# Kernel tuning notes

Measured on AMD Instinct MI355X. Metric: run time of the kernel, lower is better.

Reference implementation:

```python
import jax, jax.numpy as jnp
import numpy as np

V, D, NL = 50257, 768, 12
DI, DS, DC, DTR = 1536, 16, 4, 48  # d_inner, d_state, d_conv, dt_rank
B, S = 2, 1024


def _mamba_layer(x, iw, cw, cb, xw, dw, db, Alog, Dp, ow):
    # x: (B,S,D)
    xz = x @ iw.T                      # (B,S,2*DI)
    xin, z = jnp.split(xz, 2, axis=-1)
    # depthwise causal conv over sequence
    xc = jax.lax.conv_general_dilated(
        jnp.transpose(xin, (0, 2, 1)), cw[:, None, :],
        window_strides=(1,), padding=[(DC - 1, 0)],
        feature_group_count=DI, dimension_numbers=('NCL', 'OIL', 'NCL'))
    xin = jax.nn.silu(jnp.transpose(xc, (0, 2, 1)) + cb)  # (B,S,DI)
    dbl = xin @ xw.T                   # (B,S,DTR+2*DS)
    dt, Bm, Cm = dbl[..., :DTR], dbl[..., DTR:DTR + DS], dbl[..., DTR + DS:]
    dt = jax.nn.softplus(dt @ dw.T + db)  # (B,S,DI)
    A = -jnp.exp(Alog)                 # (DI,DS)

    def step(h, inp):
        dt_t, B_t, C_t, x_t = inp      # (B,DI),(B,DS),(B,DS),(B,DI)
        h = h * jnp.exp(dt_t[:, :, None] * A) + (dt_t * x_t)[:, :, None] * B_t[:, None, :]
        y = jnp.einsum('bds,bs->bd', h, C_t)
        return h, y

    h0 = jnp.zeros((x.shape[0], DI, DS), dtype=x.dtype)
    xs = (jnp.transpose(dt, (1, 0, 2)), jnp.transpose(Bm, (1, 0, 2)),
          jnp.transpose(Cm, (1, 0, 2)), jnp.transpose(xin, (1, 0, 2)))
    _, ys = jax.lax.scan(step, h0, xs)
    y = jnp.transpose(ys, (1, 0, 2)) + xin * Dp  # (B,S,DI)
    y = y * jax.nn.silu(z)
    return y @ ow.T                    # (B,S,D)


def _layernorm(x, w, b):
    mu = jnp.mean(x, axis=-1, keepdims=True)
    var = jnp.mean(jnp.square(x - mu), axis=-1, keepdims=True)
    return (x - mu) * jax.lax.rsqrt(var + 1e-5) * w + b


def setup_inputs() -> dict:
    key = jax.random.key(0)
    ks = jax.random.split(key, 10)
    s = 0.02
    input_ids = jax.random.randint(ks[0], (B, S), 0, V)
    emb = jax.random.normal(ks[1], (V, D), jnp.float32) * s
    in_proj_w = jax.random.normal(ks[2], (NL, 2 * DI, D), jnp.float32) * s
    conv_w = jax.random.normal(ks[3], (NL, DI, DC), jnp.float32) * 0.2
    conv_b = jnp.zeros((NL, DI), jnp.float32)
    x_proj_w = jax.random.normal(ks[4], (NL, DTR + 2 * DS, DI), jnp.float32) * s
    dt_proj_w = jax.random.normal(ks[5], (NL, DI, DTR), jnp.float32) * (DTR ** -0.5)
    dt_proj_b = jax.random.normal(ks[6], (NL, DI), jnp.float32) * 0.1 - 4.0
    A_log = jnp.broadcast_to(jnp.log(jnp.arange(1, DS + 1, dtype=jnp.float32)), (NL, DI, DS)) + 0.0
    D_param = jnp.ones((NL, DI), jnp.float32)
    out_proj_w = jax.random.normal(ks[7], (NL, D, DI), jnp.float32) * s
    norm_w = jnp.ones((D,), jnp.float32)
    norm_b = jnp.zeros((D,), jnp.float32)
    return {"input_ids": input_ids, "emb": emb, "in_proj_w": in_proj_w,
            "conv_w": conv_w, "conv_b": conv_b, "x_proj_w": x_proj_w,
            "dt_proj_w": dt_proj_w, "dt_proj_b": dt_proj_b, "A_log": A_log,
            "D_param": D_param, "out_proj_w": out_proj_w,
            "norm_w": norm_w, "norm_b": norm_b}


def reference(input_ids, emb, in_proj_w, conv_w, conv_b, x_proj_w, dt_proj_w,
              dt_proj_b, A_log, D_param, out_proj_w, norm_w, norm_b):
    x = emb[input_ids] * (D ** 0.5)    # (B,S,D)
    for i in range(NL):
        x = _mamba_layer(x, in_proj_w[i], conv_w[i], conv_b[i], x_proj_w[i],
                         dt_proj_w[i], dt_proj_b[i], A_log[i], D_param[i], out_proj_w[i])
    x = _layernorm(x, norm_w, norm_b)
    return x @ emb.T                   # tied lm_head: (B,S,V)
```

## Files before the change

### kernel.cpp

```cpp
#include <hip/hip_runtime.h>
#include <hip/hip_bf16.h>

#define DI 1536
#define DS 16
#define DC 4
#define DTR 48
#define NB 2
#define SL 1024
#define DM 768
#define NLAYER 12
#define VOCAB 50257
#define ROWS (NB*SL)
#define CCH 32
#define CLEN (SL/CCH)
#define NBIG (DI+32)

typedef __attribute__((ext_vector_type(8))) short bf16x8;
typedef __attribute__((ext_vector_type(4))) short short4v;
typedef __attribute__((ext_vector_type(4))) float f32x4;

__device__ inline short f2bf(float f) {
    unsigned u = __builtin_bit_cast(unsigned, f);
    unsigned r = (u + 0x7fffu + ((u >> 16) & 1u)) >> 16;
    return (short)r;
}

__device__ __forceinline__ void gl_lds16(const void* g, void* l) {
    __builtin_amdgcn_global_load_lds(
        (const __attribute__((address_space(1))) unsigned int*)g,
        (__attribute__((address_space(3))) unsigned int*)l, 16, 0, 0);
}

__global__ __launch_bounds__(256) void cvt_bf16_k(const float* __restrict__ src,
                                                  unsigned short* __restrict__ dst,
                                                  int n4) {
    int i = blockIdx.x * 256 + threadIdx.x;
    if (i >= n4) return;
    float4 v = *reinterpret_cast<const float4*>(src + (size_t)i * 4);
    short4v o;
    o[0] = f2bf(v.x); o[1] = f2bf(v.y); o[2] = f2bf(v.z); o[3] = f2bf(v.w);
    *reinterpret_cast<short4v*>(dst + (size_t)i * 4) = o;
}

__global__ __launch_bounds__(256) void wc_k(
    const float* __restrict__ dtw_all,
    const float* __restrict__ xpw_all,
    unsigned short* __restrict__ wbig)
{
    int l = blockIdx.z;
    const float* dtw = dtw_all + (size_t)l * DI * DTR;
    const float* xpw = xpw_all + (size_t)l * 80 * DI;
    unsigned short* wb = wbig + (size_t)l * NBIG * DI;
    int tid = threadIdx.x;
    if (blockIdx.y == 12) {
        if (blockIdx.x == 0) {
            for (int idx = tid; idx < 32 * DI; idx += 256) {
                int rr = idx / DI, k = idx - rr * DI;
                wb[(size_t)(DI + rr) * DI + k] =
                    (unsigned short)f2bf(xpw[(size_t)(48 + rr) * DI + k]);
            }
        }
        return;
    }
    __shared__ float sd[128 * 48];
    __shared__ float sx[48 * 128];
    int d0 = blockIdx.y * 128, k0 = blockIdx.x * 128;
    for (int idx = tid; idx < 128 * 48; idx += 256) {
        int r = idx / 48, j = idx - r * 48;
        sd[idx] = dtw[(size_t)(d0 + r) * DTR + j];
    }
    for (int idx = tid; idx < 48 * 128; idx += 256) {
        int j = idx / 128, k = idx - j * 128;
        sx[idx] = xpw[(size_t)j * DI + k0 + k];
    }
    __syncthreads();
    int tx = tid & 15, ty = tid >> 4;
    float acc[8][8] = {};
    for (int j = 0; j < 48; ++j) {
        float a[8], w[8];
        #pragma unroll
        for (int i = 0; i < 8; ++i) a[i] = sd[(ty * 8 + i) * 48 + j];
        #pragma unroll
        for (int i = 0; i < 8; ++i) w[i] = sx[j * 128 + tx * 8 + i];
        #pragma unroll
        for (int i = 0; i < 8; ++i)
            #pragma unroll
            for (int jj = 0; jj < 8; ++jj)
                acc[i][jj] += a[i] * w[jj];
    }
    for (int i = 0; i < 8; ++i)
        for (int jj = 0; jj < 8; ++jj)
            wb[(size_t)(d0 + ty * 8 + i) * DI + k0 + tx * 8 + jj] =
                (unsigned short)f2bf(acc[i][jj]);
}

__global__ __launch_bounds__(256) void embed_k(const int* __restrict__ ids,
                                               const float* __restrict__ emb,
                                               unsigned short* __restrict__ xbf) {
    int i = blockIdx.x * 256 + threadIdx.x;
    if (i >= ROWS * DM) return;
    int row = i / DM;
    int c = i - row * DM;
    xbf[i] = (unsigned short)f2bf(emb[(size_t)ids[row] * DM + c] * 27.712812921102035f);
}

template<int MT, int BKT, int OUT, bool NT>
__global__ __launch_bounds__(256) void gemm_bf16(
    const unsigned short* __restrict__ A, int lda,
    const unsigned short* __restrict__ W, int ldw,
    float* __restrict__ C, unsigned short* __restrict__ Cbf, int ldc,
    int GY, int N, int K,
    const float* __restrict__ bias, float* __restrict__ aux)
{
    constexpr int CPR  = BKT / 8;
    constexpr int ACA  = MT  * BKT / 2048;
    constexpr int ACW  = 128 * BKT / 2048;
    constexpr int KSUB = BKT / 32;
    constexpr int MFR  = MT / 32;
    constexpr int SMEM_AB = (MT + 128) * BKT * 2;
    constexpr int SMEM_NT = 32 * 132 * 4;
    constexpr int SMEM_SZ = ((OUT == 0 && NT) && SMEM_AB < SMEM_NT) ? SMEM_NT : SMEM_AB;
    __shared__ __align__(16) char smem[SMEM_SZ];
    short* As = (short*)smem;
    short* Ws = (short*)(smem + MT * BKT * 2);

    const int tid  = threadIdx.x;
    const int lane = tid & 63;
    const int wid  = tid >> 6;
    const int wr   = wid >> 1, wc = wid & 1;

    const int nwg = gridDim.x;
    const int q = nwg >> 3, rm = nwg & 7;
    const int xcd = blockIdx.x & 7, bidx = blockIdx.x >> 3;
    const int wg = (xcd < rm ? xcd * (q + 1) : rm * (q + 1) + (xcd - rm) * q) + bidx;
    const int row0 = (wg % GY) * MT;
    const int col0 = (wg / GY) * 128;

    const unsigned short* gA[ACA];
    const unsigned short* gW[ACW];
    #pragma unroll
    for (int i = 0; i < ACA; ++i) {
        int cid = i * 256 + tid;
        int r = cid / CPR, c = cid % CPR;
        int sz = (BKT == 32) ? ((r >> 1) & 3) : (r & 7);
        gA[i] = A + (size_t)(row0 + r) * lda + ((c ^ sz) * 8);
    }
    #pragma unroll
    for (int i = 0; i < ACW; ++i) {
        int cid = i * 256 + tid;
        int r = cid / CPR, c = cid % CPR;
        int sz = (BKT == 32) ? ((r >> 1) & 3) : (r & 7);
        int rg = col0 + r; if (rg > N - 1) rg = N - 1;
        gW[i] = W + (size_t)rg * ldw + ((c ^ sz) * 8);
    }

    const int arow = wr * (MT / 2) + (lane & 15);
    const int brow = wc * 64 + (lane & 15);
    const int szA = (BKT == 32) ? ((arow >> 1) & 3) : (arow & 7);
    const int szB = (BKT == 32) ? ((brow >> 1) & 3) : (brow & 7);
    const int hi = lane >> 4;

    f32x4 acc[MFR][4] = {};

    for (int k0 = 0; k0 < K; k0 += BKT) {
        #pragma unroll
        for (int i = 0; i < ACA; ++i) {
            gl_lds16(gA[i], &As[(size_t)(i * 256 + wid * 64) * 8]);
            gA[i] += BKT;
        }
        #pragma unroll
        for (int i = 0; i < ACW; ++i) {
            gl_lds16(gW[i], &Ws[(size_t)(i * 256 + wid * 64) * 8]);
            gW[i] += BKT;
        }
        __syncthreads();

        #pragma unroll
        for (int ks = 0; ks < KSUB; ++ks) {
            const int kc = hi + 4 * ks;
            bf16x8 a[MFR], b[4];
            #pragma unroll
            for (int mf = 0; mf < MFR; ++mf)
                a[mf] = *reinterpret_cast<const bf16x8*>(
                    &As[(arow + mf * 16) * BKT + ((kc ^ szA) * 8)]);
            #pragma unroll
            for (int nf = 0; nf < 4; ++nf)
                b[nf] = *reinterpret_cast<const bf16x8*>(
                    &Ws[(brow + nf * 16) * BKT + ((kc ^ szB) * 8)]);
            #pragma unroll
            for (int mf = 0; mf < MFR; ++mf)
                #pragma unroll
                for (int nf = 0; nf < 4; ++nf)
                    acc[mf][nf] = __builtin_amdgcn_mfma_f32_16x16x32_bf16(
                        a[mf], b[nf], acc[mf][nf], 0, 0, 0);
        }
        __syncthreads();
    }

    if (OUT == 0 && NT) {
        float* Cs = (float*)smem;
        #pragma unroll
        for (int mf = 0; mf < MFR; ++mf) {
            __syncthreads();
            #pragma unroll
            for (int nf = 0; nf < 4; ++nf) {
                #pragma unroll
                for (int j = 0; j < 4; ++j)
                    Cs[(wr * 16 + hi * 4 + j) * 132 + wc * 64 + nf * 16 + (lane & 15)]
                        = acc[mf][nf][j];
            }
            __syncthreads();
            #pragma unroll
            for (int rr = 0; rr < 8; ++rr) {
                int lrow = wid * 8 + rr;
                int grow = row0 + (lrow < 16 ? mf * 16 + lrow
                                             : (MT / 2) + mf * 16 + (lrow - 16));
                #pragma unroll
                for (int hf = 0; hf < 2; ++hf) {
                    int cc = col0 + hf * 64 + lane;
                    if (cc < N)
                        __builtin_nontemporal_store(
                            Cs[lrow * 132 + hf * 64 + lane],
                            &C[(size_t)grow * ldc + cc]);
                }
            }
        }
    } else {
        #pragma unroll
        for (int mf = 0; mf < MFR; ++mf) {
            #pragma unroll
            for (int nf = 0; nf < 4; ++nf) {
                int r  = row0 + wr * (MT / 2) + mf * 16 + hi * 4;
                int cc = col0 + wc * 64 + nf * 16 + (lane & 15);
                if (cc < N) {
                    f32x4 d = acc[mf][nf];
                    if (OUT == 3) {
                        if (cc < DI) {
                            float bv = bias[cc];
                            #pragma unroll
                            for (int j = 0; j < 4; ++j) {
                                float v = d[j] + bv;
                                v = (v > 20.f) ? v : log1pf(__expf(v));
                                C[(size_t)(r + j) * ldc + cc] = v;
                            }
                        } else {
                            #pragma unroll
                            for (int j = 0; j < 4; ++j)
                                aux[(size_t)(r + j) * 32 + (cc - DI)] = d[j];
                        }
                    } else {
                        #pragma unroll
                        for (int j = 0; j < 4; ++j) {
                            C[(size_t)(r + j) * ldc + cc] = d[j];
                            if (OUT == 1)
                                Cbf[(size_t)(r + j) * ldc + cc] =
                                    (unsigned short)f2bf(d[j]);
                        }
                    }
                }
            }
        }
    }
}

__global__ __launch_bounds__(256) void conv_silu_k(
    const float* __restrict__ xz, const float* __restrict__ cw,
    const float* __restrict__ cb, float* __restrict__ xinf,
    unsigned short* __restrict__ xinb)
{
    int i = blockIdx.x * 256 + threadIdx.x;
    if (i >= ROWS * DI) return;
    int row = i / DI;
    int c = i - row * DI;
    int t = row & (SL - 1);
    int b = row >> 10;
    float acc = cb[c];
    const float* base = xz + (size_t)(b * SL) * (2 * DI) + c;
    #pragma unroll
    for (int k = 0; k < DC; ++k) {
        int tt = t + k - (DC - 1);
        if (tt >= 0) acc += base[(size_t)tt * (2 * DI)] * cw[c * DC + k];
    }
    float v = acc / (1.f + __expf(-acc));
    xinf[i] = v;
    xinb[i] = (unsigned short)f2bf(v);
}

__global__ __launch_bounds__(256) void scan_phase1(
    const float* __restrict__ dt,
    const float* __restrict__ bc,
    const float* __restrict__ xin,
    const float* __restrict__ Alog,
    float* __restrict__ hend,
    float* __restrict__ eprod)
{
    int blk = blockIdx.x;
    int c = blk % CCH;
    int tmp = blk / CCH;
    int dblk = tmp % (DI / 16);
    int b = tmp / (DI / 16);
    int s = threadIdx.x & 15;
    int d = dblk * 16 + (threadIdx.x >> 4);
    float A = -__expf(Alog[d * DS + s]);
    float h = 0.f, P = 1.f;
    const int rowbase = b * SL + c * CLEN;
    #pragma unroll 4
    for (int t = 0; t < CLEN; ++t) {
        int r = rowbase + t;
        float dtv = dt[(size_t)r * DI + d];
        float xv  = xin[(size_t)r * DI + d];
        float Bv  = bc[(size_t)r * 32 + s];
        float e = __expf(dtv * A);
        h = h * e + dtv * xv * Bv;
        P *= e;
    }
    size_t idx = ((size_t)(b * CCH + c) * DI + d) * DS + s;
    hend[idx]  = h;
    eprod[idx] = P;
}

__global__ __launch_bounds__(256) void scan_phase3(
    const float* __restrict__ dt,
    const float* __restrict__ bc,
    const float* __restrict__ xin,
    const float* __restrict__ xz,
    const float* __restrict__ Alog,
    const float* __restrict__ Dp,
    const float* __restrict__ hend,
    const float* __restrict__ eprod,
    unsigned short* __restrict__ ybf)
{
    int blk = blockIdx.x;
    int c = blk % CCH;
    int tmp = blk / CCH;
    int dblk = tmp % (DI / 16);
    int b = tmp / (DI / 16);
    int s = threadIdx.x & 15;
    int d = dblk * 16 + (threadIdx.x >> 4);
    float A = -__expf(Alog[d * DS + s]);
    float Dv = Dp[d];

    float h = 0.f;
    const size_t pbase = ((size_t)b * CCH * DI + d) * DS + s;
    for (int j = 0; j < c; ++j) {
        size_t idx = pbase + (size_t)j * (DI * DS);
        h = h * eprod[idx] + hend[idx];
    }

    const int rowbase = b * SL + c * CLEN;
    #pragma unroll 2
    for (int t = 0; t < CLEN; ++t) {
        int r = rowbase + t;
        float dtv = dt[(size_t)r * DI + d];
        float xv  = xin[(size_t)r * DI + d];
        float Bv  = bc[(size_t)r * 32 + s];
        float Cv  = bc[(size_t)r * 32 + 16 + s];
        float e = __expf(dtv * A);
        h = h * e + dtv * xv * Bv;
        float p = h * Cv;
        p += __shfl_xor(p, 1, 64);
        p += __shfl_xor(p, 2, 64);
        p += __shfl_xor(p, 4, 64);
        p += __shfl_xor(p, 8, 64);
        if (s == 0) {
            float z = xz[(size_t)r * (2 * DI) + DI + d];
            float yv = (p + xv * Dv) * (z / (1.f + __expf(-z)));
            ybf[(size_t)r * DI + d] = (unsigned short)f2bf(yv);
        }
    }
}

__global__ __launch_bounds__(256) void ln_k(
    const float* __restrict__ x, const float* __restrict__ w,
    const float* __restrict__ b, unsigned short* __restrict__ o)
{
    int row = blockIdx.x;
    int tid = threadIdx.x;
    const float* xr = x + (size_t)row * DM;
    float v0 = xr[tid], v1 = xr[tid + 256], v2 = xr[tid + 512];
    float s = v0 + v1 + v2;
    #pragma unroll
    for (int off = 1; off < 64; off <<= 1) s += __shfl_xor(s, off, 64);
    __shared__ float red[4];
    __shared__ float red2[4];
    int wid = tid >> 6, lane = tid & 63;
    if (lane == 0) red[wid] = s;
    __syncthreads();
    float mu = (red[0] + red[1] + red[2] + red[3]) * (1.f / 768.f);
    float d0 = v0 - mu, d1 = v1 - mu, d2 = v2 - mu;
    float q = d0 * d0 + d1 * d1 + d2 * d2;
    #pragma unroll
    for (int off = 1; off < 64; off <<= 1) q += __shfl_xor(q, off, 64);
    if (lane == 0) red2[wid] = q;
    __syncthreads();
    float var = (red2[0] + red2[1] + red2[2] + red2[3]) * (1.f / 768.f);
    float rs = rsqrtf(var + 1e-5f);
    o[(size_t)row * DM + tid]       = (unsigned short)f2bf(d0 * rs * w[tid]       + b[tid]);
    o[(size_t)row * DM + tid + 256] = (unsigned short)f2bf(d1 * rs * w[tid + 256] + b[tid + 256]);
    o[(size_t)row * DM + tid + 512] = (unsigned short)f2bf(d2 * rs * w[tid + 512] + b[tid + 512]);
}

extern "C" void kernel_launch(void* const* d_in, const int* in_sizes, int n_in,
                              void* d_out, int out_size, void* d_ws, size_t ws_size,
                              hipStream_t stream) {
    const int*   ids        = (const int*)d_in[0];
    const float* emb        = (const float*)d_in[1];
    const float* in_proj_w  = (const float*)d_in[2];
    const float* conv_w     = (const float*)d_in[3];
    const float* conv_b     = (const float*)d_in[4];
    const float* x_proj_w   = (const float*)d_in[5];
    const float* dt_proj_w  = (const float*)d_in[6];
    const float* dt_proj_b  = (const float*)d_in[7];
    const float* A_log      = (const float*)d_in[8];
    const float* D_param    = (const float*)d_in[9];
    const float* out_proj_w = (const float*)d_in[10];
    const float* norm_w     = (const float*)d_in[11];
    const float* norm_b     = (const float*)d_in[12];
    float* out = (float*)d_out;

    char* base = (char*)d_ws;
    size_t off = 0;
    auto alloc_f = [&](size_t n) { float* p = (float*)(base + off); off += n * 4; return p; };
    auto alloc_u = [&](size_t n) { unsigned short* p = (unsigned short*)(base + off); off += n * 2; return p; };

    float* x     = alloc_f((size_t)ROWS * DM);
    float* xz    = alloc_f((size_t)ROWS * 2 * DI);
    float* xinf  = alloc_f((size_t)ROWS * DI);
    float* bc    = alloc_f((size_t)ROWS * 32);
    float* dt    = alloc_f((size_t)ROWS * DI);
    float* hend  = alloc_f((size_t)NB * CCH * DI * DS);
    float* eprod = alloc_f((size_t)NB * CCH * DI * DS);
    unsigned short* xbf   = alloc_u((size_t)ROWS * DM);
    unsigned short* ybf   = alloc_u((size_t)ROWS * DI);
    unsigned short* xinb  = alloc_u((size_t)ROWS * DI);
    unsigned short* xlnbf = alloc_u((size_t)ROWS * DM);
    unsigned short* inw_bf = alloc_u((size_t)NLAYER * 2 * DI * DM);
    unsigned short* ow_bf  = alloc_u((size_t)NLAYER * DM * DI);
    unsigned short* wbig  = alloc_u((size_t)NLAYER * NBIG * DI);
    unsigned short* emb_bf = alloc_u((size_t)VOCAB * DM);
    (void)ws_size;

    {
        int n4a = NLAYER * 2 * DI * DM / 4;
        cvt_bf16_k<<<(n4a + 255) / 256, 256, 0, stream>>>(in_proj_w, inw_bf, n4a);
        int n4b = NLAYER * DM * DI / 4;
        cvt_bf16_k<<<(n4b + 255) / 256, 256, 0, stream>>>(out_proj_w, ow_bf, n4b);
        wc_k<<<dim3(12, 13, NLAYER), 256, 0, stream>>>(dt_proj_w, x_proj_w, wbig);
        int n4e = VOCAB * DM / 4;
        cvt_bf16_k<<<(n4e + 255) / 256, 256, 0, stream>>>(emb, emb_bf, n4e);
    }

    embed_k<<<(ROWS * DM + 255) / 256, 256, 0, stream>>>(ids, emb, xbf);

    const int scan_grid = NB * (DI / 16) * CCH;

    for (int i = 0; i < NLAYER; ++i) {
        const float* cw  = conv_w  + (size_t)i * DI * DC;
        const float* cb  = conv_b  + (size_t)i * DI;
        const float* dtb = dt_proj_b + (size_t)i * DI;
        const float* Al  = A_log   + (size_t)i * DI * DS;
        const float* Dpar= D_param + (size_t)i * DI;

        const unsigned short* inw = inw_bf + (size_t)i * 2 * DI * DM;
        gemm_bf16<64, 64, 0, false><<<24 * 32, 256, 0, stream>>>(
            xbf, DM, inw, DM, xz, nullptr, 2 * DI, 32, 2 * DI, DM, nullptr, nullptr);

        conv_silu_k<<<(ROWS * DI) / 256, 256, 0, stream>>>(xz, cw, cb, xinf, xinb);

        const unsigned short* wb = wbig + (size_t)i * NBIG * DI;
        gemm_bf16<64, 64, 3, false><<<13 * 32, 256, 0, stream>>>(
            xinb, DI, wb, DI, dt, nullptr, DI, 32, NBIG, DI, dtb, bc);

        scan_phase1<<<scan_grid, 256, 0, stream>>>(dt, bc, xinf, Al, hend, eprod);
        scan_phase3<<<scan_grid, 256, 0, stream>>>(dt, bc, xinf, xz, Al, Dpar,
                                                   hend, eprod, ybf);

        const unsigned short* ow = ow_bf + (size_t)i * DM * DI;
        gemm_bf16<64, 64, 1, false><<<6 * 32, 256, 0, stream>>>(
            ybf, DI, ow, DI, x, xbf, DM, 32, DM, DI, nullptr, nullptr);
    }

    ln_k<<<ROWS, 256, 0, stream>>>(x, norm_w, norm_b, xlnbf);
    gemm_bf16<128, 32, 0, true><<<393 * 16, 256, 0, stream>>>(
        xlnbf, DM, emb_bf, DM, out, nullptr, VOCAB, 16, VOCAB, DM, nullptr, nullptr);
}
```

Measured before the change: 3.408 ms.

## Double-buffer LDS tiles in bf16 GEMM with a single barrier per k-step

Rewrites the GEMM main loop to use two LDS buffers. The next k-tile's global-to-LDS copies are issued before the MFMAs run on the current tile, and only one barrier is kept per iteration. The K tile is fixed at 32 for every GEMM, so the layer GEMMs drop from 64 to 32 and the template parameter goes away. The goal is to hide global load latency behind compute. The cost is more LDS per block and more loop iterations and barriers for the layer GEMMs.

```diff
diff --git a/kernel.cpp b/kernel.cpp
--- a/kernel.cpp
+++ b/kernel.cpp
@@ -104,7 +104,7 @@
     xbf[i] = (unsigned short)f2bf(emb[(size_t)ids[row] * DM + c] * 27.712812921102035f);
 }
 
-template<int MT, int BKT, int OUT, bool NT>
+template<int MT, int OUT, bool NTST>
 __global__ __launch_bounds__(256) void gemm_bf16(
     const unsigned short* __restrict__ A, int lda,
     const unsigned short* __restrict__ W, int ldw,
@@ -112,17 +112,13 @@
     int GY, int N, int K,
     const float* __restrict__ bias, float* __restrict__ aux)
 {
-    constexpr int CPR  = BKT / 8;
-    constexpr int ACA  = MT  * BKT / 2048;
-    constexpr int ACW  = 128 * BKT / 2048;
-    constexpr int KSUB = BKT / 32;
-    constexpr int MFR  = MT / 32;
-    constexpr int SMEM_AB = (MT + 128) * BKT * 2;
-    constexpr int SMEM_NT = 32 * 132 * 4;
-    constexpr int SMEM_SZ = ((OUT == 0 && NT) && SMEM_AB < SMEM_NT) ? SMEM_NT : SMEM_AB;
-    __shared__ __align__(16) char smem[SMEM_SZ];
-    short* As = (short*)smem;
-    short* Ws = (short*)(smem + MT * BKT * 2);
+    constexpr int BKT = 32;
+    constexpr int CPR = BKT / 8;
+    constexpr int ACA = MT * CPR / 256;
+    constexpr int ACW = 128 * CPR / 256;
+    constexpr int MFR = MT / 32;
+    constexpr int BUFS = (MT + 128) * BKT;
+    __shared__ __align__(16) short smem[2 * BUFS];
 
     const int tid  = threadIdx.x;
     const int lane = tid & 63;
@@ -142,62 +138,69 @@
     for (int i = 0; i < ACA; ++i) {
         int cid = i * 256 + tid;
         int r = cid / CPR, c = cid % CPR;
-        int sz = (BKT == 32) ? ((r >> 1) & 3) : (r & 7);
-        gA[i] = A + (size_t)(row0 + r) * lda + ((c ^ sz) * 8);
+        gA[i] = A + (size_t)(row0 + r) * lda + ((c ^ ((r >> 1) & 3)) * 8);
     }
     #pragma unroll
     for (int i = 0; i < ACW; ++i) {
         int cid = i * 256 + tid;
         int r = cid / CPR, c = cid % CPR;
-        int sz = (BKT == 32) ? ((r >> 1) & 3) : (r & 7);
         int rg = col0 + r; if (rg > N - 1) rg = N - 1;
-        gW[i] = W + (size_t)rg * ldw + ((c ^ sz) * 8);
+        gW[i] = W + (size_t)rg * ldw + ((c ^ ((r >> 1) & 3)) * 8);
     }
 
     const int arow = wr * (MT / 2) + (lane & 15);
     const int brow = wc * 64 + (lane & 15);
-    const int szA = (BKT == 32) ? ((arow >> 1) & 3) : (arow & 7);
-    const int szB = (BKT == 32) ? ((brow >> 1) & 3) : (brow & 7);
+    const int szA = (arow >> 1) & 3;
+    const int szB = (brow >> 1) & 3;
     const int hi = lane >> 4;
 
+    auto STAGE = [&](int buf) {
+        short* As = smem + buf * BUFS;
+        short* Ws = As + MT * BKT;
+        #pragma unroll
+        for (int i = 0; i < ACA; ++i) {
+            gl_lds16(gA[i], &As[(i * 256 + wid * 64) * 8]);
+            gA[i] += BKT;
+        }
+        #pragma unroll
+        for (int i = 0; i < ACW; ++i) {
+            gl_lds16(gW[i], &Ws[(i * 256 + wid * 64) * 8]);
+            gW[i] += BKT;
+        }
+    };
+
     f32x4 acc[MFR][4] = {};
 
-    for (int k0 = 0; k0 < K; k0 += BKT) {
-        #pragma unroll
-        for (int i = 0; i < ACA; ++i) {
-            gl_lds16(gA[i], &As[(size_t)(i * 256 + wid * 64) * 8]);
-            gA[i] += BKT;
-        }
-        #pragma unroll
-        for (int i = 0; i < ACW; ++i) {
-            gl_lds16(gW[i], &Ws[(size_t)(i * 256 + wid * 64) * 8]);
-            gW[i] += BKT;
-        }
-        __syncthreads();
-
-        #pragma unroll
-        for (int ks = 0; ks < KSUB; ++ks) {
-            const int kc = hi + 4 * ks;
-            bf16x8 a[MFR], b[4];
-            #pragma unroll
-            for (int mf = 0; mf < MFR; ++mf)
-                a[mf] = *reinterpret_cast<const bf16x8*>(
-                    &As[(arow + mf * 16) * BKT + ((kc ^ szA) * 8)]);
+    STAGE(0);
+    __syncthreads();
+
+    const int ntiles = K / BKT;
+    for (int t = 0; t < ntiles; ++t) {
+        const int cur = t & 1;
+        if (t + 1 < ntiles) STAGE(cur ^ 1);
+
+        const short* As = smem + cur * BUFS;
+        const short* Ws = As + MT * BKT;
+        bf16x8 a[MFR], b[4];
+        #pragma unroll
+        for (int mf = 0; mf < MFR; ++mf)
+            a[mf] = *reinterpret_cast<const bf16x8*>(
+                &As[(arow + mf * 16) * BKT + ((hi ^ szA) * 8)]);
+        #pragma unroll
+        for (int nf = 0; nf < 4; ++nf)
+            b[nf] = *reinterpret_cast<const bf16x8*>(
+                &Ws[(brow + nf * 16) * BKT + ((hi ^ szB) * 8)]);
+        #pragma unroll
+        for (int mf = 0; mf < MFR; ++mf)
             #pragma unroll
             for (int nf = 0; nf < 4; ++nf)
-                b[nf] = *reinterpret_cast<const bf16x8*>(
-                    &Ws[(brow + nf * 16) * BKT + ((kc ^ szB) * 8)]);
-            #pragma unroll
-            for (int mf = 0; mf < MFR; ++mf)
-                #pragma unroll
-                for (int nf = 0; nf < 4; ++nf)
-                    acc[mf][nf] = __builtin_amdgcn_mfma_f32_16x16x32_bf16(
-                        a[mf], b[nf], acc[mf][nf], 0, 0, 0);
-        }
+                acc[mf][nf] = __builtin_amdgcn_mfma_f32_16x16x32_bf16(
+                    a[mf], b[nf], acc[mf][nf], 0, 0, 0);
+
         __syncthreads();
     }
 
-    if (OUT == 0 && NT) {
+    if (OUT == 0 && NTST) {
         float* Cs = (float*)smem;
         #pragma unroll
         for (int mf = 0; mf < MFR; ++mf) {
@@ -462,13 +465,13 @@
         const float* Dpar= D_param + (size_t)i * DI;
 
         const unsigned short* inw = inw_bf + (size_t)i * 2 * DI * DM;
-        gemm_bf16<64, 64, 0, false><<<24 * 32, 256, 0, stream>>>(
+        gemm_bf16<64, 0, false><<<24 * 32, 256, 0, stream>>>(
             xbf, DM, inw, DM, xz, nullptr, 2 * DI, 32, 2 * DI, DM, nullptr, nullptr);
 
         conv_silu_k<<<(ROWS * DI) / 256, 256, 0, stream>>>(xz, cw, cb, xinf, xinb);
 
         const unsigned short* wb = wbig + (size_t)i * NBIG * DI;
-        gemm_bf16<64, 64, 3, false><<<13 * 32, 256, 0, stream>>>(
+        gemm_bf16<64, 3, false><<<13 * 32, 256, 0, stream>>>(
             xinb, DI, wb, DI, dt, nullptr, DI, 32, NBIG, DI, dtb, bc);
 
         scan_phase1<<<scan_grid, 256, 0, stream>>>(dt, bc, xinf, Al, hend, eprod);
@@ -476,11 +479,11 @@
                                                    hend, eprod, ybf);
 
         const unsigned short* ow = ow_bf + (size_t)i * DM * DI;
-        gemm_bf16<64, 64, 1, false><<<6 * 32, 256, 0, stream>>>(
+        gemm_bf16<64, 1, false><<<6 * 32, 256, 0, stream>>>(
             ybf, DI, ow, DI, x, xbf, DM, 32, DM, DI, nullptr, nullptr);
     }
 
     ln_k<<<ROWS, 256, 0, stream>>>(x, norm_w, norm_b, xlnbf);
-    gemm_bf16<128, 32, 0, true><<<393 * 16, 256, 0, stream>>>(
+    gemm_bf16<128, 0, true><<<393 * 16, 256, 0, stream>>>(
         xlnbf, DM, emb_bf, DM, out, nullptr, VOCAB, 16, VOCAB, DM, nullptr, nullptr);
 }
```

New measurement: 3.388 ms. About the same (-0.6%).
